# Optimization experiments

Measured on AMD Instinct MI355X. Metric: run time of the kernel, lower is better.

The kernel has to match this reference:

```python
import jax, jax.numpy as jnp
import numpy as np
from jax import lax

R = 1          # guided filter radius
EPS = 1e-05    # regularizer


def _box_filter(x, r):
    # Separable moving-average, VALID padding (matches Keras DepthwiseConv2D default).
    # Original applies filter_y (k,1) first, then filter_x (1,k).
    k = 2 * r + 1
    c = x.shape[-1]
    ky = jnp.full((k, 1, 1, c), 1.0 / k, x.dtype)  # HWIO depthwise kernel
    kx = jnp.full((1, k, 1, c), 1.0 / k, x.dtype)
    dn = lax.conv_dimension_numbers(x.shape, ky.shape, ('NHWC', 'HWIO', 'NHWC'))
    x = lax.conv_general_dilated(x, ky, (1, 1), 'VALID', dimension_numbers=dn,
                                 feature_group_count=c)
    x = lax.conv_general_dilated(x, kx, (1, 1), 'VALID', dimension_numbers=dn,
                                 feature_group_count=c)
    return x


def setup_inputs() -> dict:
    key = jax.random.key(0)
    k1, k2, k3 = jax.random.split(key, 3)
    lr_x = jax.random.normal(k1, (2, 270, 480, 4), jnp.float32)
    lr_y = jax.random.normal(k2, (2, 270, 480, 4), jnp.float32)
    hr_x = jax.random.normal(k3, (2, 1080, 1920, 4), jnp.float32)
    return {"lr_x": lr_x, "lr_y": lr_y, "hr_x": hr_x}


def reference(lr_x, lr_y, hr_x):
    mean_x = _box_filter(lr_x, R)                              # [B, H-2r, W-2r, C]
    mean_y = _box_filter(lr_y, R)
    cov_xy = _box_filter(lr_x * lr_y, R) - mean_x * mean_y
    var_x = _box_filter(lr_x * lr_x, R) - mean_x * mean_x
    A = cov_xy / (var_x + EPS)
    b = mean_y - A * mean_x
    B, H, W, C = hr_x.shape
    mean_A = jax.image.resize(A, (B, H, W, C), method='bilinear', antialias=False)
    mean_b = jax.image.resize(b, (B, H, W, C), method='bilinear', antialias=False)
    return mean_A * hr_x + mean_b
```

## Files before the change

### kernel.cpp

```cpp
#include <hip/hip_runtime.h>


namespace {

constexpr int LR_H = 270, LR_W = 480;
constexpr int A_H  = 268, A_W  = 478;
constexpr int HR_H = 1080, HR_W = 1920;
constexpr int BATCH = 2;
constexpr float EPS_F = 1e-5f;

constexpr int TILE_W = 256;
constexpr int NTILES = (HR_W + TILE_W - 1) / TILE_W;
constexpr int ROWS   = 8;
constexpr int ROWGRP = HR_H / ROWS;
constexpr int VCOLS  = 68;
constexpr int ACOLS  = 66;
constexpr int RSETS  = 4;

using f32x4 = __attribute__((ext_vector_type(4))) float;

__device__ __forceinline__ float4 f4add(float4 a, float4 b) {
    return make_float4(a.x + b.x, a.y + b.y, a.z + b.z, a.w + b.w);
}
__device__ __forceinline__ float4 f4sub(float4 a, float4 b) {
    return make_float4(a.x - b.x, a.y - b.y, a.z - b.z, a.w - b.w);
}
__device__ __forceinline__ float4 f4mul(float4 a, float4 b) {
    return make_float4(a.x * b.x, a.y * b.y, a.z * b.z, a.w * b.w);
}
__device__ __forceinline__ float4 f4scale(float4 a, float s) {
    return make_float4(a.x * s, a.y * s, a.z * s, a.w * s);
}
__device__ __forceinline__ float4 f4fma(float4 a, float4 b, float4 c) {
    return make_float4(fmaf(a.x, b.x, c.x), fmaf(a.y, b.y, c.y),
                       fmaf(a.z, b.z, c.z), fmaf(a.w, b.w, c.w));
}
__device__ __forceinline__ float4 f4lerp(float4 a, float4 b, float t) {
    return make_float4(fmaf(t, b.x - a.x, a.x), fmaf(t, b.y - a.y, a.y),
                       fmaf(t, b.z - a.z, a.z), fmaf(t, b.w - a.w, a.w));
}
__device__ __forceinline__ float4 f4axpy(float s, float4 v, float4 acc) {
    return make_float4(fmaf(s, v.x, acc.x), fmaf(s, v.y, acc.y),
                       fmaf(s, v.z, acc.z), fmaf(s, v.w, acc.w));
}
__device__ __forceinline__ float4 f4rcp(float4 a) {
    return make_float4(__builtin_amdgcn_rcpf(a.x), __builtin_amdgcn_rcpf(a.y),
                       __builtin_amdgcn_rcpf(a.z), __builtin_amdgcn_rcpf(a.w));
}
__device__ __forceinline__ void nt_store(float4 v, float4* p) {
    f32x4 rv = {v.x, v.y, v.z, v.w};
    __builtin_nontemporal_store(rv, (f32x4*)p);
}

}

__global__ __launch_bounds__(256) void
fgf_fused8(const float4* __restrict__ lr_x,
           const float4* __restrict__ lr_y,
           const float4* __restrict__ hr_x,
           float4* __restrict__ out) {
    __shared__ float4 vs[RSETS][4][VCOLS];
    __shared__ float4 sA4[RSETS][ACOLS];
    __shared__ float4 sB4[RSETS][ACOLS];

    int bid  = blockIdx.x;
    int tile = bid % NTILES;
    int g    = bid / NTILES;
    int rg   = g % ROWGRP;
    int b    = g / ROWGRP;
    int tid  = threadIdx.x;

    constexpr float sh_scale = (float)A_H / (float)HR_H;
    constexpr float sw_scale = (float)A_W / (float)HR_W;

    int hbase = rg * ROWS;
    int R0 = (int)floorf((hbase + 0.5f) * sh_scale - 0.5f);

    int w_start = tile * TILE_W;
    int c0 = (int)floorf((w_start + 0.5f) * sw_scale - 0.5f);

    int w = w_start + tid;
    bool valid = (w < HR_W);
    size_t hr_row0 = ((size_t)b * HR_H + hbase) * (size_t)HR_W + w;
    float4 xr[ROWS];
#pragma unroll
    for (int j = 0; j < ROWS; ++j) {
        xr[j] = valid ? hr_x[hr_row0 + (size_t)j * HR_W]
                      : make_float4(0.f, 0.f, 0.f, 0.f);
    }

    for (int t = tid; t < RSETS * VCOLS; t += 256) {
        int rs = t / VCOLS;
        int cs = t - rs * VCOLS;
        int ar = min(max(R0 + rs, 0), A_H - 1);
        int col = min(max(c0 + cs, 0), LR_W - 1);
        const float4* px = lr_x + ((size_t)b * LR_H + ar) * LR_W + col;
        const float4* py = lr_y + ((size_t)b * LR_H + ar) * LR_W + col;
        float4 sx  = make_float4(0.f, 0.f, 0.f, 0.f);
        float4 sy  = make_float4(0.f, 0.f, 0.f, 0.f);
        float4 sxy = make_float4(0.f, 0.f, 0.f, 0.f);
        float4 sxx = make_float4(0.f, 0.f, 0.f, 0.f);
#pragma unroll
        for (int dy = 0; dy < 3; ++dy) {
            float4 x = px[(size_t)dy * LR_W];
            float4 y = py[(size_t)dy * LR_W];
            sx  = f4add(sx, x);
            sy  = f4add(sy, y);
            sxy = f4fma(x, y, sxy);
            sxx = f4fma(x, x, sxx);
        }
        vs[rs][0][cs] = sx;
        vs[rs][1][cs] = sy;
        vs[rs][2][cs] = sxy;
        vs[rs][3][cs] = sxx;
    }
    __syncthreads();

    constexpr float inv9 = 1.0f / 9.0f;
    for (int t = tid; t < RSETS * ACOLS; t += 256) {
        int rs = t / ACOLS;
        int sl = t - rs * ACOLS;
        int a  = min(max(c0 + sl, 0), A_W - 1);
        int bs = a - c0;
        float4 hx  = f4add(f4add(vs[rs][0][bs], vs[rs][0][bs + 1]), vs[rs][0][bs + 2]);
        float4 hy  = f4add(f4add(vs[rs][1][bs], vs[rs][1][bs + 1]), vs[rs][1][bs + 2]);
        float4 hxy = f4add(f4add(vs[rs][2][bs], vs[rs][2][bs + 1]), vs[rs][2][bs + 2]);
        float4 hxx = f4add(f4add(vs[rs][3][bs], vs[rs][3][bs + 1]), vs[rs][3][bs + 2]);
        float4 mx  = f4scale(hx, inv9);
        float4 my  = f4scale(hy, inv9);
        float4 cov = f4sub(f4scale(hxy, inv9), f4mul(mx, my));
        float4 var = f4sub(f4scale(hxx, inv9), f4mul(mx, mx));
        float4 A = f4mul(cov, f4rcp(make_float4(var.x + EPS_F, var.y + EPS_F,
                                                var.z + EPS_F, var.w + EPS_F)));
        float4 bb = f4sub(my, f4mul(A, mx));
        sA4[rs][sl] = A;
        sB4[rs][sl] = bb;
    }
    __syncthreads();

    float sw = (w + 0.5f) * sw_scale - 0.5f;
    float fw = floorf(sw);
    float tw = sw - fw;
    int wi = min((int)fw - c0, ACOLS - 2);

    float4 hA0 = f4lerp(sA4[0][wi], sA4[0][wi + 1], tw);
    float4 hB0 = f4lerp(sB4[0][wi], sB4[0][wi + 1], tw);
    float4 hA1 = f4lerp(sA4[1][wi], sA4[1][wi + 1], tw);
    float4 hB1 = f4lerp(sB4[1][wi], sB4[1][wi + 1], tw);
    float4 hA2 = f4lerp(sA4[2][wi], sA4[2][wi + 1], tw);
    float4 hB2 = f4lerp(sB4[2][wi], sB4[2][wi + 1], tw);
    float4 hA3 = f4lerp(sA4[3][wi], sA4[3][wi + 1], tw);
    float4 hB3 = f4lerp(sB4[3][wi], sB4[3][wi + 1], tw);

    if (valid) {
#pragma unroll
        for (int j = 0; j < ROWS; ++j) {
            float shj = (hbase + j + 0.5f) * sh_scale - 0.5f;
            float t = shj - (float)R0;
            float w0 = fmaxf(1.f - fabsf(t - 0.f), 0.f);
            float w1 = fmaxf(1.f - fabsf(t - 1.f), 0.f);
            float w2 = fmaxf(1.f - fabsf(t - 2.f), 0.f);
            float w3 = fmaxf(1.f - fabsf(t - 3.f), 0.f);

            float4 aI = f4axpy(w3, hA3, f4axpy(w2, hA2,
                        f4axpy(w1, hA1, f4scale(hA0, w0))));
            float4 bI = f4axpy(w3, hB3, f4axpy(w2, hB2,
                        f4axpy(w1, hB1, f4scale(hB0, w0))));

            nt_store(f4fma(aI, xr[j], bI), &out[hr_row0 + (size_t)j * HR_W]);
        }
    }
}

extern "C" void kernel_launch(void* const* d_in, const int* in_sizes, int n_in,
                              void* d_out, int out_size, void* d_ws, size_t ws_size,
                              hipStream_t stream) {
    const float4* lr_x = (const float4*)d_in[0];
    const float4* lr_y = (const float4*)d_in[1];
    const float4* hr_x = (const float4*)d_in[2];
    float4* out = (float4*)d_out;

    constexpr int nblocks = BATCH * ROWGRP * NTILES;
    fgf_fused8<<<nblocks, 256, 0, stream>>>(lr_x, lr_y, hr_x, out);
}
```

Baseline: 27.27 us.

## Retile to 240-wide, 5-row blocks with 3 low-res row sets

Changes the tile to 240 columns by 5 rows so tiles divide the high-res width exactly. Each block then needs only 3 low-res coefficient rows and 64 vertical-sum columns, so the strided loops become single-pass thread mappings and the vertical interpolation drops to 3 weights. Launch bounds request 8 blocks per CU. In exchange there are more blocks, 16 idle threads per block in the output phase, and more redundant low-res recomputation per output pixel.

```diff
diff --git a/kernel.cpp b/kernel.cpp
--- a/kernel.cpp
+++ b/kernel.cpp
@@ -9,13 +9,13 @@
 constexpr int BATCH = 2;
 constexpr float EPS_F = 1e-5f;
 
-constexpr int TILE_W = 256;
-constexpr int NTILES = (HR_W + TILE_W - 1) / TILE_W;
-constexpr int ROWS   = 8;
+constexpr int TILE_W = 240;
+constexpr int NTILES = HR_W / TILE_W;
+constexpr int ROWS   = 5;
 constexpr int ROWGRP = HR_H / ROWS;
-constexpr int VCOLS  = 68;
-constexpr int ACOLS  = 66;
-constexpr int RSETS  = 4;
+constexpr int VCOLS  = 64;
+constexpr int ACOLS  = 62;
+constexpr int RSETS  = 3;
 
 using f32x4 = __attribute__((ext_vector_type(4))) float;
 
@@ -54,8 +54,8 @@
 
 }
 
-__global__ __launch_bounds__(256) void
-fgf_fused8(const float4* __restrict__ lr_x,
+__global__ __launch_bounds__(256, 8) void
+fgf_fused5(const float4* __restrict__ lr_x,
            const float4* __restrict__ lr_y,
            const float4* __restrict__ hr_x,
            float4* __restrict__ out) {
@@ -64,8 +64,8 @@
     __shared__ float4 sB4[RSETS][ACOLS];
 
     int bid  = blockIdx.x;
-    int tile = bid % NTILES;
-    int g    = bid / NTILES;
+    int tile = bid & (NTILES - 1);
+    int g    = bid >> 3;
     int rg   = g % ROWGRP;
     int b    = g / ROWGRP;
     int tid  = threadIdx.x;
@@ -80,7 +80,7 @@
     int c0 = (int)floorf((w_start + 0.5f) * sw_scale - 0.5f);
 
     int w = w_start + tid;
-    bool valid = (w < HR_W);
+    bool valid = (tid < TILE_W);
     size_t hr_row0 = ((size_t)b * HR_H + hbase) * (size_t)HR_W + w;
     float4 xr[ROWS];
 #pragma unroll
@@ -89,9 +89,9 @@
                       : make_float4(0.f, 0.f, 0.f, 0.f);
     }
 
-    for (int t = tid; t < RSETS * VCOLS; t += 256) {
-        int rs = t / VCOLS;
-        int cs = t - rs * VCOLS;
+    if (tid < RSETS * VCOLS) {
+        int rs = tid >> 6;
+        int cs = tid & 63;
         int ar = min(max(R0 + rs, 0), A_H - 1);
         int col = min(max(c0 + cs, 0), LR_W - 1);
         const float4* px = lr_x + ((size_t)b * LR_H + ar) * LR_W + col;
@@ -117,55 +117,52 @@
     __syncthreads();
 
     constexpr float inv9 = 1.0f / 9.0f;
-    for (int t = tid; t < RSETS * ACOLS; t += 256) {
-        int rs = t / ACOLS;
-        int sl = t - rs * ACOLS;
-        int a  = min(max(c0 + sl, 0), A_W - 1);
-        int bs = a - c0;
-        float4 hx  = f4add(f4add(vs[rs][0][bs], vs[rs][0][bs + 1]), vs[rs][0][bs + 2]);
-        float4 hy  = f4add(f4add(vs[rs][1][bs], vs[rs][1][bs + 1]), vs[rs][1][bs + 2]);
-        float4 hxy = f4add(f4add(vs[rs][2][bs], vs[rs][2][bs + 1]), vs[rs][2][bs + 2]);
-        float4 hxx = f4add(f4add(vs[rs][3][bs], vs[rs][3][bs + 1]), vs[rs][3][bs + 2]);
-        float4 mx  = f4scale(hx, inv9);
-        float4 my  = f4scale(hy, inv9);
-        float4 cov = f4sub(f4scale(hxy, inv9), f4mul(mx, my));
-        float4 var = f4sub(f4scale(hxx, inv9), f4mul(mx, mx));
-        float4 A = f4mul(cov, f4rcp(make_float4(var.x + EPS_F, var.y + EPS_F,
-                                                var.z + EPS_F, var.w + EPS_F)));
-        float4 bb = f4sub(my, f4mul(A, mx));
-        sA4[rs][sl] = A;
-        sB4[rs][sl] = bb;
+    {
+        int rs = tid >> 6;
+        int sl = tid & 63;
+        if (rs < RSETS && sl < ACOLS) {
+            int a  = min(max(c0 + sl, 0), A_W - 1);
+            int bs = a - c0;
+            float4 hx  = f4add(f4add(vs[rs][0][bs], vs[rs][0][bs + 1]), vs[rs][0][bs + 2]);
+            float4 hy  = f4add(f4add(vs[rs][1][bs], vs[rs][1][bs + 1]), vs[rs][1][bs + 2]);
+            float4 hxy = f4add(f4add(vs[rs][2][bs], vs[rs][2][bs + 1]), vs[rs][2][bs + 2]);
+            float4 hxx = f4add(f4add(vs[rs][3][bs], vs[rs][3][bs + 1]), vs[rs][3][bs + 2]);
+            float4 mx  = f4scale(hx, inv9);
+            float4 my  = f4scale(hy, inv9);
+            float4 cov = f4sub(f4scale(hxy, inv9), f4mul(mx, my));
+            float4 var = f4sub(f4scale(hxx, inv9), f4mul(mx, mx));
+            float4 A = f4mul(cov, f4rcp(make_float4(var.x + EPS_F, var.y + EPS_F,
+                                                    var.z + EPS_F, var.w + EPS_F)));
+            float4 bb = f4sub(my, f4mul(A, mx));
+            sA4[rs][sl] = A;
+            sB4[rs][sl] = bb;
+        }
     }
     __syncthreads();
 
-    float sw = (w + 0.5f) * sw_scale - 0.5f;
-    float fw = floorf(sw);
-    float tw = sw - fw;
-    int wi = min((int)fw - c0, ACOLS - 2);
+    if (valid) {
+        float sw = (w + 0.5f) * sw_scale - 0.5f;
+        float fw = floorf(sw);
+        float tw = sw - fw;
+        int wi = min((int)fw - c0, ACOLS - 2);
 
-    float4 hA0 = f4lerp(sA4[0][wi], sA4[0][wi + 1], tw);
-    float4 hB0 = f4lerp(sB4[0][wi], sB4[0][wi + 1], tw);
-    float4 hA1 = f4lerp(sA4[1][wi], sA4[1][wi + 1], tw);
-    float4 hB1 = f4lerp(sB4[1][wi], sB4[1][wi + 1], tw);
-    float4 hA2 = f4lerp(sA4[2][wi], sA4[2][wi + 1], tw);
-    float4 hB2 = f4lerp(sB4[2][wi], sB4[2][wi + 1], tw);
-    float4 hA3 = f4lerp(sA4[3][wi], sA4[3][wi + 1], tw);
-    float4 hB3 = f4lerp(sB4[3][wi], sB4[3][wi + 1], tw);
+        float4 hA0 = f4lerp(sA4[0][wi], sA4[0][wi + 1], tw);
+        float4 hB0 = f4lerp(sB4[0][wi], sB4[0][wi + 1], tw);
+        float4 hA1 = f4lerp(sA4[1][wi], sA4[1][wi + 1], tw);
+        float4 hB1 = f4lerp(sB4[1][wi], sB4[1][wi + 1], tw);
+        float4 hA2 = f4lerp(sA4[2][wi], sA4[2][wi + 1], tw);
+        float4 hB2 = f4lerp(sB4[2][wi], sB4[2][wi + 1], tw);
 
-    if (valid) {
 #pragma unroll
         for (int j = 0; j < ROWS; ++j) {
             float shj = (hbase + j + 0.5f) * sh_scale - 0.5f;
             float t = shj - (float)R0;
-            float w0 = fmaxf(1.f - fabsf(t - 0.f), 0.f);
-            float w1 = fmaxf(1.f - fabsf(t - 1.f), 0.f);
-            float w2 = fmaxf(1.f - fabsf(t - 2.f), 0.f);
-            float w3 = fmaxf(1.f - fabsf(t - 3.f), 0.f);
+            float w0 = fmaxf(1.f - t, 0.f);
+            float w1 = 1.f - fabsf(t - 1.f);
+            float w2 = fmaxf(t - 1.f, 0.f);
 
-            float4 aI = f4axpy(w3, hA3, f4axpy(w2, hA2,
-                        f4axpy(w1, hA1, f4scale(hA0, w0))));
-            float4 bI = f4axpy(w3, hB3, f4axpy(w2, hB2,
-                        f4axpy(w1, hB1, f4scale(hB0, w0))));
+            float4 aI = f4axpy(w2, hA2, f4axpy(w1, hA1, f4scale(hA0, w0)));
+            float4 bI = f4axpy(w2, hB2, f4axpy(w1, hB1, f4scale(hB0, w0)));
 
             nt_store(f4fma(aI, xr[j], bI), &out[hr_row0 + (size_t)j * HR_W]);
         }
@@ -181,5 +178,5 @@
     float4* out = (float4*)d_out;
 
     constexpr int nblocks = BATCH * ROWGRP * NTILES;
-    fgf_fused8<<<nblocks, 256, 0, stream>>>(lr_x, lr_y, hr_x, out);
+    fgf_fused5<<<nblocks, 256, 0, stream>>>(lr_x, lr_y, hr_x, out);
 }
```

Result: slower. 29.91 us (+9.7%).
